# Kernel optimization log

Hardware: AMD Instinct MI355X
Metric: run time of the kernel (lower is better)

The kernel has to match this reference:

```python
import jax, jax.numpy as jnp
import numpy as np

B, S, D = 2, 2048, 2048
NH = 16
HD = D // NH  # 128
MAX_POS = 4096
ROPE_THETA = 10000.0


def rotate_half(x):
    x1, x2 = x[..., : x.shape[-1] // 2], x[..., x.shape[-1] // 2 :]
    return jnp.concatenate((-x2, x1), axis=-1)


def rope_tables(dtype=jnp.float32):
    inv_freq = 1.0 / (ROPE_THETA ** (jnp.arange(0, HD, 2, dtype=jnp.float32) / HD))
    t = jnp.arange(MAX_POS, dtype=jnp.float32)
    freqs = jnp.outer(t, inv_freq)              # [MAX_POS, HD/2]
    emb = jnp.concatenate((freqs, freqs), axis=-1)  # [MAX_POS, HD]
    return jnp.cos(emb).astype(dtype), jnp.sin(emb).astype(dtype)


def setup_inputs() -> dict:
    key = jax.random.key(0)
    ks = jax.random.split(key, 9)
    sc = 0.02
    return {
        "hidden_states": jax.random.normal(ks[0], (B, S, D), jnp.float32),
        "position_ids": jnp.arange(B * S, dtype=jnp.int32).reshape(B, S),
        "Wq": jax.random.normal(ks[1], (D, D), jnp.float32) * sc,
        "bq": jax.random.normal(ks[2], (D,), jnp.float32) * sc,
        "Wk": jax.random.normal(ks[3], (D, D), jnp.float32) * sc,
        "bk": jax.random.normal(ks[4], (D,), jnp.float32) * sc,
        "Wv": jax.random.normal(ks[5], (D, D), jnp.float32) * sc,
        "bv": jax.random.normal(ks[6], (D,), jnp.float32) * sc,
        "Wo": jax.random.normal(ks[7], (D, D), jnp.float32) * sc,
    }


def reference(hidden_states, position_ids, Wq, bq, Wk, bk, Wv, bv, Wo):
    b, s, _ = hidden_states.shape
    # projections (torch Linear: x @ W.T + b)
    q = (hidden_states @ Wq.T + bq).reshape(b, s, NH, HD).transpose(0, 2, 1, 3)
    k = (hidden_states @ Wk.T + bk).reshape(b, s, NH, HD).transpose(0, 2, 1, 3)
    v = (hidden_states @ Wv.T + bv).reshape(b, s, NH, HD).transpose(0, 2, 1, 3)
    # RoPE
    cos_t, sin_t = rope_tables(hidden_states.dtype)
    cos = cos_t[position_ids][:, None, :, :]  # [B,1,S,HD]
    sin = sin_t[position_ids][:, None, :, :]
    q = q * cos + rotate_half(q) * sin
    k = k * cos + rotate_half(k) * sin
    # NOTE: faithful to the source bug — softmax is computed but its result is
    # discarded; the AV matmul uses the UNNORMALIZED scaled scores.
    attn_weights = jnp.einsum("bhqd,bhkd->bhqk", q, k) / (HD ** 0.5)
    _ = jax.nn.softmax(attn_weights.astype(jnp.float32), axis=-1)  # dead, as in source
    attn_output = jnp.einsum("bhqk,bhkd->bhqd", attn_weights, v)
    attn_output = attn_output.transpose(0, 2, 1, 3).reshape(b, s, D)
    return attn_output @ Wo.T
```

## Files before the change

kernel.cpp:

```cpp
#include <hip/hip_runtime.h>
#include <hip/hip_bf16.h>


typedef __attribute__((ext_vector_type(8))) short bf16x8s;
typedef __attribute__((ext_vector_type(4))) float f32x4;

__device__ __forceinline__ ushort f2bf(float f) {
    union { float f; unsigned int u; } x; x.f = f;
    unsigned int u = x.u;
    unsigned int r = (u + 0x7fffu + ((u >> 16) & 1u)) >> 16;
    return (ushort)r;
}
__device__ __forceinline__ float b2f(ushort u) {
    union { unsigned int u; float f; } x; x.u = ((unsigned int)u) << 16;
    return x.f;
}

__device__ __forceinline__ void gload_lds16(const void* g, void* l) {
    __builtin_amdgcn_global_load_lds((__attribute__((address_space(1))) const void*)g,
                                     (__attribute__((address_space(3))) void*)l, 16, 0, 0);
}

template<bool BIAS, bool OBF16>
__global__ __launch_bounds__(512, 2)
void gemm256(const ushort* __restrict__ A, const ushort* __restrict__ B,
             const float* __restrict__ bias, void* __restrict__ Cv,
             int K, int lda, int ldb, int ldc,
             long sAb, long sBb, long sCb)
{
    __shared__ char smem[131072];

    int z = blockIdx.z;
    const ushort* Ab = A + (size_t)sAb * z;
    const ushort* Bb = B + (size_t)sBb * z;
    size_t Coff = (size_t)sCb * z;

    int nwgx = gridDim.x;
    int nwg = nwgx * gridDim.y;
    int wg = blockIdx.y * nwgx + blockIdx.x;
    int swz = ((nwg & 7) == 0) ? (wg & 7) * (nwg >> 3) + (wg >> 3) : wg;
    int m0 = (swz % nwgx) * 256;
    int n0 = (swz / nwgx) * 256;

    int tid = threadIdx.x;
    int l = tid & 63, wid = tid >> 6;
    int wm = (wid >> 2) * 128;
    int wn = (wid & 3) * 64;
    int lr = l & 15, lj = l >> 4;

    int offA[8], offB[4];
#pragma unroll
    for (int m = 0; m < 8; m++) {
        int r = wm + m * 16 + lr;
        offA[m] = (r >> 1) * 128 + (((((r & 1) << 2) | lj) ^ ((r >> 1) & 7)) << 4);
    }
#pragma unroll
    for (int n = 0; n < 4; n++) {
        int r = wn + n * 16 + lr;
        offB[n] = (r >> 1) * 128 + (((((r & 1) << 2) | lj) ^ ((r >> 1) & 7)) << 4);
    }

    unsigned srcA0, srcA1, srcB0, srcB1;
    int dst0 = tid * 16, dst1 = dst0 + 8192;
    {
        int c0 = tid, c1 = tid + 512;
        int pr0 = c0 >> 3, up0 = (c0 & 7) ^ (pr0 & 7);
        int r0 = (pr0 << 1) | (up0 >> 2), j0 = up0 & 3;
        int pr1 = c1 >> 3, up1 = (c1 & 7) ^ (pr1 & 7);
        int r1 = (pr1 << 1) | (up1 >> 2), j1 = up1 & 3;
        srcA0 = (unsigned)(m0 + r0) * lda + j0 * 8;
        srcA1 = (unsigned)(m0 + r1) * lda + j1 * 8;
        srcB0 = (unsigned)(n0 + r0) * ldb + j0 * 8;
        srcB1 = (unsigned)(n0 + r1) * ldb + j1 * 8;
    }

    f32x4 acc[8][4];
#pragma unroll
    for (int m = 0; m < 8; m++)
#pragma unroll
        for (int n = 0; n < 4; n++)
            acc[m][n] = (f32x4){0.f, 0.f, 0.f, 0.f};

    int NT = K >> 6;

#define STAGE_A(ldsbyte, eoff) { \
    gload_lds16(Ab + srcA0 + (eoff), smem + (ldsbyte) + dst0); \
    gload_lds16(Ab + srcA1 + (eoff), smem + (ldsbyte) + dst1); }
#define STAGE_B(ldsbyte, eoff) { \
    gload_lds16(Bb + srcB0 + (eoff), smem + (ldsbyte) + dst0); \
    gload_lds16(Bb + srcB1 + (eoff), smem + (ldsbyte) + dst1); }
#define MFMA_HALF(mb) { \
    __builtin_amdgcn_s_setprio(1); \
    _Pragma("unroll") \
    for (int m = 0; m < 4; m++) \
        _Pragma("unroll") \
        for (int n = 0; n < 4; n++) \
            acc[(mb) + m][n] = __builtin_amdgcn_mfma_f32_16x16x32_bf16( \
                af[(mb) + m], bf[n], acc[(mb) + m][n], 0, 0, 0); \
    __builtin_amdgcn_s_setprio(0); }

    STAGE_A(0, 0);
    STAGE_B(32768, 0);
    STAGE_A(16384, 32);
    STAGE_B(49152, 32);
    asm volatile("s_waitcnt vmcnt(4)" ::: "memory");
    __builtin_amdgcn_s_barrier();

    for (int t = 0; t < NT; ++t) {
        int lb = (t & 1) << 16;
        int pb = lb ^ 65536;
        bool pf = (t + 1 < NT);
        unsigned eo = (unsigned)(t + 1) * 64;
        bf16x8s af[8], bf[4];

#pragma unroll
        for (int m = 0; m < 4; m++)
            af[m] = *(const bf16x8s*)(smem + lb + offA[m]);
#pragma unroll
        for (int n = 0; n < 4; n++)
            bf[n] = *(const bf16x8s*)(smem + lb + 32768 + offB[n]);
        if (pf) STAGE_A(pb, eo);
#pragma unroll
        for (int m = 4; m < 8; m++)
            af[m] = *(const bf16x8s*)(smem + lb + offA[m]);
        asm volatile("s_waitcnt lgkmcnt(4)" ::: "memory");
        __builtin_amdgcn_sched_barrier(0);
        MFMA_HALF(0);
        asm volatile("s_waitcnt lgkmcnt(0)" ::: "memory");
        __builtin_amdgcn_sched_barrier(0);
        MFMA_HALF(4);
        if (pf) STAGE_B(pb + 32768, eo);
        if (pf) asm volatile("s_waitcnt vmcnt(4)" ::: "memory");
        else    asm volatile("s_waitcnt vmcnt(0)" ::: "memory");
        __builtin_amdgcn_s_barrier();

#pragma unroll
        for (int m = 0; m < 4; m++)
            af[m] = *(const bf16x8s*)(smem + lb + 16384 + offA[m]);
#pragma unroll
        for (int n = 0; n < 4; n++)
            bf[n] = *(const bf16x8s*)(smem + lb + 49152 + offB[n]);
        if (pf) STAGE_A(pb + 16384, eo + 32);
#pragma unroll
        for (int m = 4; m < 8; m++)
            af[m] = *(const bf16x8s*)(smem + lb + 16384 + offA[m]);
        asm volatile("s_waitcnt lgkmcnt(4)" ::: "memory");
        __builtin_amdgcn_sched_barrier(0);
        MFMA_HALF(0);
        asm volatile("s_waitcnt lgkmcnt(0)" ::: "memory");
        __builtin_amdgcn_sched_barrier(0);
        MFMA_HALF(4);
        if (pf) {
            STAGE_B(pb + 49152, eo + 32);
            asm volatile("s_waitcnt vmcnt(4)" ::: "memory");
            __builtin_amdgcn_s_barrier();
        }
    }
#undef STAGE_A
#undef STAGE_B
#undef MFMA_HALF

    int rr = lj * 4;
#pragma unroll
    for (int m = 0; m < 8; m++) {
#pragma unroll
        for (int n = 0; n < 4; n++) {
            int gr = m0 + wm + m * 16 + rr;
            int gc = n0 + wn + n * 16 + lr;
            float bv = BIAS ? bias[gc] : 0.f;
#pragma unroll
            for (int r = 0; r < 4; r++) {
                float v = acc[m][n][r] + bv;
                size_t off = Coff + (size_t)(gr + r) * ldc + gc;
                if (OBF16) ((ushort*)Cv)[off] = f2bf(v);
                else       ((float*)Cv)[off]  = v;
            }
        }
    }
}

template<bool BIAS, bool OBF16, int BN>
__global__ __launch_bounds__(256)
void gemm_nt(const ushort* __restrict__ A, const ushort* __restrict__ B,
             const float* __restrict__ bias, void* __restrict__ Cv,
             int K, int lda, int ldb, int ldc, int ZH,
             long sAb, long sAh, long sBb, long sBh, long sCb, long sCh)
{
    __shared__ ushort As[128 * 32];
    __shared__ ushort Bs[BN * 32];

    int z  = blockIdx.z;
    int zb = z / ZH, zh = z - zb * ZH;
    const ushort* Ab = A + (size_t)(sAb * zb + sAh * zh);
    const ushort* Bb = B + (size_t)(sBb * zb + sBh * zh);
    size_t Coff = (size_t)(sCb * zb + sCh * zh);

    int m0 = blockIdx.x * 128, n0 = blockIdx.y * BN;
    int t = threadIdx.x;
    int l = t & 63, w = t >> 6;
    int wm, wn;
    if (BN == 128) { wm = (w >> 1) * 64; wn = (w & 1) * 64; }
    else           { wm = w * 32;        wn = 0; }
    constexpr int FM = (BN == 128) ? 4 : 2;
    constexpr int FN = 4;
    int lr = l & 15, lk = (l >> 4) * 8;

    f32x4 acc[FM][FN];
#pragma unroll
    for (int i = 0; i < FM; i++)
#pragma unroll
        for (int j = 0; j < FN; j++)
            acc[i][j] = (f32x4){0.f, 0.f, 0.f, 0.f};

    int c0 = t, c1 = t + 256;
    int r0 = c0 >> 2, k0c = (c0 & 3) * 8;
    int r1 = c1 >> 2, k1c = (c1 & 3) * 8;

    for (int kt = 0; kt < K; kt += 32) {
        __syncthreads();
        gload_lds16(Ab + (size_t)(m0 + r0) * lda + kt + k0c, &As[c0 * 8]);
        gload_lds16(Ab + (size_t)(m0 + r1) * lda + kt + k1c, &As[c1 * 8]);
        gload_lds16(Bb + (size_t)(n0 + r0) * ldb + kt + k0c, &Bs[c0 * 8]);
        if (BN == 128)
            gload_lds16(Bb + (size_t)(n0 + r1) * ldb + kt + k1c, &Bs[c1 * 8]);
        __syncthreads();

        bf16x8s af[FM], bf[FN];
#pragma unroll
        for (int i = 0; i < FM; i++)
            af[i] = *(const bf16x8s*)&As[(wm + i * 16 + lr) * 32 + lk];
#pragma unroll
        for (int i = 0; i < FN; i++)
            bf[i] = *(const bf16x8s*)&Bs[(wn + i * 16 + lr) * 32 + lk];
#pragma unroll
        for (int mi = 0; mi < FM; mi++)
#pragma unroll
            for (int ni = 0; ni < FN; ni++)
                acc[mi][ni] = __builtin_amdgcn_mfma_f32_16x16x32_bf16(
                    af[mi], bf[ni], acc[mi][ni], 0, 0, 0);
    }

    int rr = (l >> 4) * 4;
#pragma unroll
    for (int mi = 0; mi < FM; mi++) {
#pragma unroll
        for (int ni = 0; ni < FN; ni++) {
            int gr = m0 + wm + mi * 16 + rr;
            int gc = n0 + wn + ni * 16 + lr;
            float bv = BIAS ? bias[gc] : 0.f;
#pragma unroll
            for (int r = 0; r < 4; r++) {
                float v = acc[mi][ni][r] + bv;
                size_t off = Coff + (size_t)(gr + r) * ldc + gc;
                if (OBF16) ((ushort*)Cv)[off] = f2bf(v);
                else       ((float*)Cv)[off]  = v;
            }
        }
    }
}

__global__ __launch_bounds__(256)
void rope_qk(ushort* __restrict__ QKV, const int* __restrict__ pos,
             ushort* __restrict__ QB)
{
    int tid = blockIdx.x * 256 + threadIdx.x;
    int row = tid >> 7;
    int r = tid & 127;
    int h = r >> 3, j = r & 7;
    int d0 = j * 8;
    float p = (float)pos[row];
    size_t qb = (size_t)row * 6144 + h * 128 + d0;

    bf16x8s q1 = *(const bf16x8s*)&QKV[qb];
    bf16x8s q2 = *(const bf16x8s*)&QKV[qb + 64];
    bf16x8s k1 = *(const bf16x8s*)&QKV[qb + 2048];
    bf16x8s k2 = *(const bf16x8s*)&QKV[qb + 2048 + 64];
    bf16x8s oq1, oq2, ok1, ok2;
#pragma unroll
    for (int i = 0; i < 8; i++) {
        float d = (float)(d0 + i);
        float ang = p * exp2f(d * (-13.287712379549449f / 64.0f));
        float s, c;
        sincosf(ang, &s, &c);
        float a = b2f((ushort)q1[i]), b = b2f((ushort)q2[i]);
        oq1[i] = (short)f2bf(a * c - b * s);
        oq2[i] = (short)f2bf(b * c + a * s);
        float e = b2f((ushort)k1[i]), f = b2f((ushort)k2[i]);
        ok1[i] = (short)f2bf(e * c - f * s);
        ok2[i] = (short)f2bf(f * c + e * s);
    }
    size_t ob = (size_t)row * 2048 + h * 128 + d0;
    *(bf16x8s*)&QB[ob]      = oq1;
    *(bf16x8s*)&QB[ob + 64] = oq2;
    *(bf16x8s*)&QKV[qb + 2048]      = ok1;
    *(bf16x8s*)&QKV[qb + 2048 + 64] = ok2;
}

__global__ __launch_bounds__(256)
void ktv_partial(const ushort* __restrict__ QKV, float* __restrict__ part)
{
    int bh = blockIdx.x;
    int b = bh >> 4, h = bh & 15;
    int s0 = blockIdx.y * 128;
    const ushort* Kp = QKV + (size_t)(b * 2048 + s0) * 6144 + 2048 + h * 128;
    const ushort* Vp = Kp + 2048;

    __shared__ ushort Ks[32][128];
    __shared__ ushort Vs[32][128];

    int t = threadIdx.x;
    int tx = t & 15, ty = t >> 4;
    float acc[8][8];
#pragma unroll
    for (int i = 0; i < 8; i++)
#pragma unroll
        for (int j = 0; j < 8; j++) acc[i][j] = 0.f;

    for (int sb = 0; sb < 128; sb += 32) {
        __syncthreads();
#pragma unroll
        for (int i = 0; i < 2; i++) {
            int idx = t + i * 256;
            int rw = idx >> 4, c8 = (idx & 15) * 8;
            *(bf16x8s*)&Ks[rw][c8] = *(const bf16x8s*)&Kp[(size_t)(sb + rw) * 6144 + c8];
            *(bf16x8s*)&Vs[rw][c8] = *(const bf16x8s*)&Vp[(size_t)(sb + rw) * 6144 + c8];
        }
        __syncthreads();
        for (int ss = 0; ss < 32; ss++) {
            bf16x8s kvv = *(const bf16x8s*)&Ks[ss][tx * 8];
            bf16x8s vvv = *(const bf16x8s*)&Vs[ss][ty * 8];
            float kv[8], vv[8];
#pragma unroll
            for (int i = 0; i < 8; i++) { kv[i] = b2f((ushort)kvv[i]); vv[i] = b2f((ushort)vvv[i]); }
#pragma unroll
            for (int i = 0; i < 8; i++)
#pragma unroll
                for (int j = 0; j < 8; j++)
                    acc[i][j] += kv[i] * vv[j];
        }
    }
    float* pp = part + ((size_t)blockIdx.y * 32 + bh) * 16384;
#pragma unroll
    for (int i = 0; i < 8; i++)
#pragma unroll
        for (int j = 0; j < 8; j++)
            pp[(tx * 8 + i) * 128 + (ty * 8 + j)] = acc[i][j];
}

__global__ __launch_bounds__(256)
void reduce_ktv(const float* __restrict__ part, ushort* __restrict__ Mb)
{
    int i = blockIdx.x * 256 + threadIdx.x;
    float s = 0.f;
#pragma unroll
    for (int p = 0; p < 16; p++) s += part[(size_t)p * 524288 + i];
    Mb[i] = f2bf(s * 0.08838834764831845f);
}

__global__ __launch_bounds__(256)
void conv_f32_bf16(const float* __restrict__ in, ushort* __restrict__ out, int n4)
{
    int i = blockIdx.x * 256 + threadIdx.x;
    if (i >= n4) return;
    float4 v = ((const float4*)in)[i];
    ushort4 o;
    o.x = f2bf(v.x); o.y = f2bf(v.y); o.z = f2bf(v.z); o.w = f2bf(v.w);
    ((ushort4*)out)[i] = o;
}

__global__ __launch_bounds__(256)
void conv_weights(const float* __restrict__ w0, const float* __restrict__ w1,
                  const float* __restrict__ w2, const float* __restrict__ w3,
                  ushort* __restrict__ qkv, ushort* __restrict__ wo)
{
    int i = blockIdx.x * 256 + threadIdx.x;
    int id = i >> 20;
    int off = i & 1048575;
    const float* src = (id == 0) ? w0 : (id == 1) ? w1 : (id == 2) ? w2 : w3;
    float4 v = ((const float4*)src)[off];
    ushort4 o;
    o.x = f2bf(v.x); o.y = f2bf(v.y); o.z = f2bf(v.z); o.w = f2bf(v.w);
    if (id < 3) ((ushort4*)qkv)[(size_t)id * 1048576 + off] = o;
    else        ((ushort4*)wo)[off] = o;
}

__global__ __launch_bounds__(256)
void pack_bias(const float* __restrict__ bq, const float* __restrict__ bk,
               const float* __restrict__ bv, float* __restrict__ bqkv)
{
    int i = blockIdx.x * 256 + threadIdx.x;
    float v = (i < 2048) ? bq[i] : (i < 4096) ? bk[i - 2048] : bv[i - 4096];
    bqkv[i] = v;
}

extern "C" void kernel_launch(void* const* d_in, const int* in_sizes, int n_in,
                              void* d_out, int out_size, void* d_ws, size_t ws_size,
                              hipStream_t stream)
{
    const float* hs = (const float*)d_in[0];
    const int*  pos = (const int*)d_in[1];
    const float* Wq = (const float*)d_in[2];
    const float* bq = (const float*)d_in[3];
    const float* Wk = (const float*)d_in[4];
    const float* bk = (const float*)d_in[5];
    const float* Wv = (const float*)d_in[6];
    const float* bv = (const float*)d_in[7];
    const float* Wo = (const float*)d_in[8];
    float* out = (float*)d_out;
    char* ws = (char*)d_ws;

    ushort* HSB  = (ushort*)(ws + 0);
    ushort* QB   = (ushort*)(ws + 0);
    ushort* WQKV = (ushort*)(ws + 16777216);
    ushort* NT   = (ushort*)(ws + 16777216);
    ushort* WOB  = (ushort*)(ws + 41943040);
    float*  BQKV = (float*)(ws + 50331648);
    ushort* QKVB = (ushort*)(ws + 50356224);
    ushort* MB   = (ushort*)(ws + 100687872);
    float*  PART = out;

    dim3 blk(256);

    conv_f32_bf16<<<8192, blk, 0, stream>>>(hs, HSB, 2097152);
    conv_weights<<<16384, blk, 0, stream>>>(Wq, Wk, Wv, Wo, WQKV, WOB);
    pack_bias<<<24, blk, 0, stream>>>(bq, bk, bv, BQKV);

    gemm256<true, true><<<dim3(16, 24, 1), dim3(512), 0, stream>>>(
        HSB, WQKV, BQKV, QKVB, 2048, 2048, 2048, 6144, 0, 0, 0);

    rope_qk<<<2048, blk, 0, stream>>>(QKVB, pos, QB);

    ktv_partial<<<dim3(32, 16, 1), blk, 0, stream>>>(QKVB, PART);
    reduce_ktv<<<2048, blk, 0, stream>>>(PART, MB);

    gemm_nt<false, true, 128><<<dim3(16, 1, 32), blk, 0, stream>>>(
        WOB, MB, nullptr, NT, 128, 2048, 128, 2048, 16,
        0, 128, 262144, 16384, 4194304, 128);

    gemm256<false, false><<<dim3(8, 8, 2), dim3(512), 0, stream>>>(
        QB, NT, nullptr, out, 2048, 2048, 2048, 2048,
        4194304, 4194304, 4194304);
}
```

Baseline: 382.1 us.

## Split-K the final GEMM and fuse K RoPE into the KᵀV partial kernel

The final 2048x2048x2048 GEMM per batch now runs as a two-way split-K. This doubles the grid from 128 to 256 workgroups to fill more CUs. The second K-half writes to a scratch buffer, and a new add_out kernel sums it into the output. Separately, RoPE on K moves from the standalone rope kernel into ktv_partial, applied in LDS after the load. This removes a global K write and re-read, at the cost of an extra barrier and duplicated sincos work. The risk is the extra fp32 partial write plus the add pass, which is roughly 32 MB of traffic.

```diff
diff --git a/kernel.cpp b/kernel.cpp
--- a/kernel.cpp
+++ b/kernel.cpp
@@ -25,15 +25,18 @@
 __global__ __launch_bounds__(512, 2)
 void gemm256(const ushort* __restrict__ A, const ushort* __restrict__ B,
              const float* __restrict__ bias, void* __restrict__ Cv,
-             int K, int lda, int ldb, int ldc,
+             void* __restrict__ CvAlt, int kspan, int nsplit,
+             int lda, int ldb, int ldc,
              long sAb, long sBb, long sCb)
 {
     __shared__ char smem[131072];
 
     int z = blockIdx.z;
-    const ushort* Ab = A + (size_t)sAb * z;
-    const ushort* Bb = B + (size_t)sBb * z;
-    size_t Coff = (size_t)sCb * z;
+    int zb = z / nsplit, half = z - zb * nsplit;
+    const ushort* Ab = A + (size_t)sAb * zb + (size_t)half * kspan;
+    const ushort* Bb = B + (size_t)sBb * zb + (size_t)half * kspan;
+    void* Cdst = half ? CvAlt : Cv;
+    size_t Coff = (size_t)sCb * zb;
 
     int nwgx = gridDim.x;
     int nwg = nwgx * gridDim.y;
@@ -81,7 +84,7 @@
         for (int n = 0; n < 4; n++)
             acc[m][n] = (f32x4){0.f, 0.f, 0.f, 0.f};
 
-    int NT = K >> 6;
+    int NT = kspan >> 6;
 
 #define STAGE_A(ldsbyte, eoff) { \
     gload_lds16(Ab + srcA0 + (eoff), smem + (ldsbyte) + dst0); \
@@ -172,8 +175,8 @@
             for (int r = 0; r < 4; r++) {
                 float v = acc[m][n][r] + bv;
                 size_t off = Coff + (size_t)(gr + r) * ldc + gc;
-                if (OBF16) ((ushort*)Cv)[off] = f2bf(v);
-                else       ((float*)Cv)[off]  = v;
+                if (OBF16) ((ushort*)Cdst)[off] = f2bf(v);
+                else       ((float*)Cdst)[off]  = v;
             }
         }
     }
@@ -260,8 +263,8 @@
 }
 
 __global__ __launch_bounds__(256)
-void rope_qk(ushort* __restrict__ QKV, const int* __restrict__ pos,
-             ushort* __restrict__ QB)
+void rope_q(const ushort* __restrict__ QKV, const int* __restrict__ pos,
+            ushort* __restrict__ QB)
 {
     int tid = blockIdx.x * 256 + threadIdx.x;
     int row = tid >> 7;
@@ -273,9 +276,7 @@
 
     bf16x8s q1 = *(const bf16x8s*)&QKV[qb];
     bf16x8s q2 = *(const bf16x8s*)&QKV[qb + 64];
-    bf16x8s k1 = *(const bf16x8s*)&QKV[qb + 2048];
-    bf16x8s k2 = *(const bf16x8s*)&QKV[qb + 2048 + 64];
-    bf16x8s oq1, oq2, ok1, ok2;
+    bf16x8s oq1, oq2;
 #pragma unroll
     for (int i = 0; i < 8; i++) {
         float d = (float)(d0 + i);
@@ -285,19 +286,15 @@
         float a = b2f((ushort)q1[i]), b = b2f((ushort)q2[i]);
         oq1[i] = (short)f2bf(a * c - b * s);
         oq2[i] = (short)f2bf(b * c + a * s);
-        float e = b2f((ushort)k1[i]), f = b2f((ushort)k2[i]);
-        ok1[i] = (short)f2bf(e * c - f * s);
-        ok2[i] = (short)f2bf(f * c + e * s);
     }
     size_t ob = (size_t)row * 2048 + h * 128 + d0;
     *(bf16x8s*)&QB[ob]      = oq1;
     *(bf16x8s*)&QB[ob + 64] = oq2;
-    *(bf16x8s*)&QKV[qb + 2048]      = ok1;
-    *(bf16x8s*)&QKV[qb + 2048 + 64] = ok2;
-}
-
-__global__ __launch_bounds__(256)
-void ktv_partial(const ushort* __restrict__ QKV, float* __restrict__ part)
+}
+
+__global__ __launch_bounds__(256)
+void ktv_partial(const ushort* __restrict__ QKV, const int* __restrict__ pos,
+                 float* __restrict__ part)
 {
     int bh = blockIdx.x;
     int b = bh >> 4, h = bh & 15;
@@ -316,6 +313,8 @@
 #pragma unroll
         for (int j = 0; j < 8; j++) acc[i][j] = 0.f;
 
+    int rw_r = t >> 3, d0_r = (t & 7) * 8;
+
     for (int sb = 0; sb < 128; sb += 32) {
         __syncthreads();
 #pragma unroll
@@ -326,6 +325,25 @@
             *(bf16x8s*)&Vs[rw][c8] = *(const bf16x8s*)&Vp[(size_t)(sb + rw) * 6144 + c8];
         }
         __syncthreads();
+        {
+            float p = (float)pos[b * 2048 + s0 + sb + rw_r];
+            bf16x8s k1 = *(const bf16x8s*)&Ks[rw_r][d0_r];
+            bf16x8s k2 = *(const bf16x8s*)&Ks[rw_r][d0_r + 64];
+            bf16x8s o1, o2;
+#pragma unroll
+            for (int i = 0; i < 8; i++) {
+                float d = (float)(d0_r + i);
+                float ang = p * exp2f(d * (-13.287712379549449f / 64.0f));
+                float s, c;
+                sincosf(ang, &s, &c);
+                float e = b2f((ushort)k1[i]), f = b2f((ushort)k2[i]);
+                o1[i] = (short)f2bf(e * c - f * s);
+                o2[i] = (short)f2bf(f * c + e * s);
+            }
+            *(bf16x8s*)&Ks[rw_r][d0_r]      = o1;
+            *(bf16x8s*)&Ks[rw_r][d0_r + 64] = o2;
+        }
+        __syncthreads();
         for (int ss = 0; ss < 32; ss++) {
             bf16x8s kvv = *(const bf16x8s*)&Ks[ss][tx * 8];
             bf16x8s vvv = *(const bf16x8s*)&Vs[ss][ty * 8];
@@ -355,6 +373,16 @@
 #pragma unroll
     for (int p = 0; p < 16; p++) s += part[(size_t)p * 524288 + i];
     Mb[i] = f2bf(s * 0.08838834764831845f);
+}
+
+__global__ __launch_bounds__(256)
+void add_out(float* __restrict__ out, const float* __restrict__ p1)
+{
+    int i = blockIdx.x * 256 + threadIdx.x;
+    float4 a = ((const float4*)out)[i];
+    float4 b = ((const float4*)p1)[i];
+    a.x += b.x; a.y += b.y; a.z += b.z; a.w += b.w;
+    ((float4*)out)[i] = a;
 }
 
 __global__ __launch_bounds__(256)
@@ -416,6 +444,7 @@
     ushort* WOB  = (ushort*)(ws + 41943040);
     float*  BQKV = (float*)(ws + 50331648);
     ushort* QKVB = (ushort*)(ws + 50356224);
+    float*  P1   = (float*)(ws + 50356224);
     ushort* MB   = (ushort*)(ws + 100687872);
     float*  PART = out;
 
@@ -426,18 +455,20 @@
     pack_bias<<<24, blk, 0, stream>>>(bq, bk, bv, BQKV);
 
     gemm256<true, true><<<dim3(16, 24, 1), dim3(512), 0, stream>>>(
-        HSB, WQKV, BQKV, QKVB, 2048, 2048, 2048, 6144, 0, 0, 0);
-
-    rope_qk<<<2048, blk, 0, stream>>>(QKVB, pos, QB);
-
-    ktv_partial<<<dim3(32, 16, 1), blk, 0, stream>>>(QKVB, PART);
+        HSB, WQKV, BQKV, QKVB, QKVB, 2048, 1, 2048, 2048, 6144, 0, 0, 0);
+
+    rope_q<<<2048, blk, 0, stream>>>(QKVB, pos, QB);
+
+    ktv_partial<<<dim3(32, 16, 1), blk, 0, stream>>>(QKVB, pos, PART);
     reduce_ktv<<<2048, blk, 0, stream>>>(PART, MB);
 
     gemm_nt<false, true, 128><<<dim3(16, 1, 32), blk, 0, stream>>>(
         WOB, MB, nullptr, NT, 128, 2048, 128, 2048, 16,
         0, 128, 262144, 16384, 4194304, 128);
 
-    gemm256<false, false><<<dim3(8, 8, 2), dim3(512), 0, stream>>>(
-        QB, NT, nullptr, out, 2048, 2048, 2048, 2048,
+    gemm256<false, false><<<dim3(8, 8, 4), dim3(512), 0, stream>>>(
+        QB, NT, nullptr, out, P1, 1024, 2, 2048, 2048, 2048,
         4194304, 4194304, 4194304);
-}
+
+    add_out<<<8192, blk, 0, stream>>>(out, P1);
+}
```

After: 391.9 us. 1.03x slower.
